# Optimization experiments

Hardware: AMD Instinct MI355X
Metric: run time of the kernel (lower is better)

The kernel has to match this reference:

```python
import jax, jax.numpy as jnp
import numpy as np

N_NODES = 10000
N_EDGES = 160000
F = 128
NRB = 32


def setup_inputs() -> dict:
    key = jax.random.key(0)
    ks = jax.random.split(key, 20)
    inp = {
        "s": jax.random.normal(ks[0], (N_NODES, F), jnp.float32),
        "v": jax.random.normal(ks[1], (N_NODES, 3, F), jnp.float32),
        "radial_embeddings_1": jax.random.normal(ks[2], (N_EDGES, NRB), jnp.float32),
        "radial_embeddings_2": jax.random.normal(ks[3], (N_EDGES, NRB), jnp.float32),
        "radial_embeddings_3": jax.random.normal(ks[4], (N_EDGES, NRB), jnp.float32),
        "f_cut_1": jax.random.uniform(ks[5], (N_EDGES,), jnp.float32),
        "f_cut_2": jax.random.uniform(ks[6], (N_EDGES,), jnp.float32),
        "f_cut_3": jax.random.uniform(ks[7], (N_EDGES,), jnp.float32),
        "unit_vectors_1": jax.random.normal(ks[8], (N_EDGES, 3), jnp.float32),
        "unit_vectors_2": jax.random.normal(ks[9], (N_EDGES, 3), jnp.float32),
        "unit_vectors_3": jax.random.normal(ks[10], (N_EDGES, 3), jnp.float32),
        "edge_index": jax.random.randint(ks[11], (2, N_EDGES), 0, N_NODES, jnp.int64),
    }
    # parameters (Linear uses y = x @ W.T + b; we store transposed for x @ W)
    sc1 = 1.0 / np.sqrt(F)
    sc2 = 1.0 / np.sqrt(NRB)
    inp["W1"] = jax.random.uniform(ks[12], (F, F), jnp.float32, -sc1, sc1)
    inp["b1"] = jax.random.uniform(ks[13], (F,), jnp.float32, -sc1, sc1)
    inp["W2"] = jax.random.uniform(ks[14], (F, 8 * F), jnp.float32, -sc1, sc1)
    inp["b2"] = jax.random.uniform(ks[15], (8 * F,), jnp.float32, -sc1, sc1)
    inp["Wr"] = jax.random.uniform(ks[16], (NRB, 8 * F), jnp.float32, -sc2, sc2)
    inp["br"] = jax.random.uniform(ks[17], (8 * F,), jnp.float32, -sc2, sc2)
    return inp


def reference(s, v, radial_embeddings_1, radial_embeddings_2, radial_embeddings_3,
              f_cut_1, f_cut_2, f_cut_3,
              unit_vectors_1, unit_vectors_2, unit_vectors_3,
              edge_index, W1, b1, W2, b2, Wr, br):
    idx_i, idx_j = edge_index[0], edge_index[1]
    n_nodes = s.shape[0]
    nf = W1.shape[0]

    # phi = Linear(F,F) -> SiLU -> Linear(F,8F)   [N, 8F]
    phi = jax.nn.silu(s @ W1 + b1) @ W2 + b2

    # shared-weight radial filter over 3 branches  [E, 8F]
    W = ((radial_embeddings_1 @ Wr + br) * f_cut_1[:, None]
         + (radial_embeddings_2 @ Wr + br) * f_cut_2[:, None]
         + (radial_embeddings_3 @ Wr + br) * f_cut_3[:, None])

    x = phi[idx_j] * W                                    # [E, 8F]
    x_s, x_vv, x_vs1, x_vs2, x_vs3, x_vc1, x_vc2, x_vc3 = jnp.split(x, 8, axis=-1)

    ds = jax.ops.segment_sum(x_s, idx_i, num_segments=n_nodes)

    vj = v[idx_j]                                         # [E, 3, F]
    ex = lambda a: a[:, None, :]                          # [E,1,F] broadcast over xyz
    cr = lambda u: jnp.cross(vj, u[..., None], axis=1)    # [E, 3, F]

    x_v = (vj * ex(x_vv)
           + ex(x_vs1) * unit_vectors_1[..., None]
           + ex(x_vs2) * unit_vectors_2[..., None]
           + ex(x_vs3) * unit_vectors_3[..., None]
           + ex(x_vc1) * cr(unit_vectors_1)
           + ex(x_vc2) * cr(unit_vectors_2)
           + ex(x_vc3) * cr(unit_vectors_3))              # [E, 3, F]

    dv = jax.ops.segment_sum(x_v, idx_i, num_segments=n_nodes)
    return (s + ds, v + dv)
```

## Files before the change

kernel.cpp:

```cpp
#include <hip/hip_runtime.h>

#define N_NODES 10000
#define N_EDGES 160000
#define MAXT     20000
#define MSG_GRID 5000

typedef __attribute__((ext_vector_type(8))) __bf16 bf16x8;
typedef __attribute__((ext_vector_type(8))) unsigned short u16x8;
typedef __attribute__((ext_vector_type(4))) float f32x4;

static __device__ __forceinline__ unsigned short f2bf(float x) {
    union { float f; unsigned u; } un;
    un.f = x;
    unsigned r = un.u + 0x7fffu + ((un.u >> 16) & 1u);
    return (unsigned short)(r >> 16);
}

static __device__ __forceinline__ float bf2f(unsigned short h) {
    union { unsigned u; float f; } un;
    un.u = ((unsigned)h) << 16;
    return un.f;
}

__global__ __launch_bounds__(256) void init_kernel(
    const float* __restrict__ s, const float* __restrict__ v,
    const int* __restrict__ eix,
    const float* __restrict__ W1, const float* __restrict__ W2,
    const float* __restrict__ Wr,
    float* __restrict__ out0, float* __restrict__ out1,
    unsigned short* __restrict__ vbf2, int* __restrict__ cnt,
    unsigned short* __restrict__ W1T, unsigned short* __restrict__ W2T,
    unsigned short* __restrict__ WrT)
{
    int tid = blockIdx.x * 256 + threadIdx.x;
    if (tid < N_NODES * 384) out1[tid] = v[tid];
    if (tid < N_NODES * 128) {
        out0[tid] = s[tid];
        int n = tid >> 7, f = tid & 127;
        ushort4 q;
        q.x = f2bf(v[(size_t)n * 384 + f]);
        q.y = f2bf(v[(size_t)n * 384 + 128 + f]);
        q.z = f2bf(v[(size_t)n * 384 + 256 + f]);
        q.w = 0;
        *reinterpret_cast<ushort4*>(vbf2 + (size_t)tid * 4) = q;
    }
    if (tid < 131072) {
        int n = tid >> 7, k = tid & 127;
        W2T[tid] = f2bf(W2[k * 1024 + n]);
    }
    if (tid < 16384) {
        int n = tid >> 7, k = tid & 127;
        W1T[tid] = f2bf(W1[k * 128 + n]);
    }
    if (tid < 32768) {
        int n = tid >> 5, k = tid & 31;
        WrT[tid] = f2bf(Wr[k * 1024 + n]);
    }
    if (tid < N_EDGES) atomicAdd(&cnt[eix[tid]], 1);
}

__global__ __launch_bounds__(1024) void scan_kernel(
    const int* __restrict__ cnt, int* __restrict__ cursor,
    int* __restrict__ tile_node, int* __restrict__ tile_e0,
    int* __restrict__ tile_cnt, int* __restrict__ ntiles)
{
    __shared__ int ws0[16], ws1[16];
    __shared__ int run0_s, run1_s;
    int t = threadIdx.x, lane = t & 63, wid = t >> 6;
    if (t == 0) { run0_s = 0; run1_s = 0; }
    __syncthreads();
    for (int base = 0; base < N_NODES; base += 1024) {
        int idx = base + t;
        int deg = (idx < N_NODES) ? cnt[idx] : 0;
        int tc = (deg + 15) >> 4;
        int x0 = deg, x1 = tc;
        #pragma unroll
        for (int o = 1; o < 64; o <<= 1) {
            int y0 = __shfl_up(x0, o), y1 = __shfl_up(x1, o);
            if (lane >= o) { x0 += y0; x1 += y1; }
        }
        if (lane == 63) { ws0[wid] = x0; ws1[wid] = x1; }
        __syncthreads();
        if (wid == 0) {
            int w0 = (lane < 16) ? ws0[lane] : 0;
            int w1 = (lane < 16) ? ws1[lane] : 0;
            #pragma unroll
            for (int o = 1; o < 16; o <<= 1) {
                int y0 = __shfl_up(w0, o), y1 = __shfl_up(w1, o);
                if (lane >= o) { w0 += y0; w1 += y1; }
            }
            if (lane < 16) { ws0[lane] = w0; ws1[lane] = w1; }
        }
        __syncthreads();
        int wb0 = wid ? ws0[wid - 1] : 0;
        int wb1 = wid ? ws1[wid - 1] : 0;
        int ex0 = run0_s + wb0 + x0 - deg;
        int ex1 = run1_s + wb1 + x1 - tc;
        if (idx < N_NODES) {
            cursor[idx] = ex0;
            for (int k = 0; k < tc; ++k) {
                tile_node[ex1 + k] = idx;
                tile_e0[ex1 + k]   = ex0 + k * 16;
                int rem = deg - k * 16;
                tile_cnt[ex1 + k]  = rem < 16 ? rem : 16;
            }
        }
        __syncthreads();
        if (t == 0) { run0_s += ws0[15]; run1_s += ws1[15]; }
        __syncthreads();
    }
    if (t == 0) *ntiles = run1_s;
}

__global__ __launch_bounds__(256) void rc_kernel(
    const float* __restrict__ R1, const float* __restrict__ R2,
    const float* __restrict__ R3,
    const float* __restrict__ f1, const float* __restrict__ f2,
    const float* __restrict__ f3,
    const int* __restrict__ eix, int* __restrict__ cursor,
    unsigned short* __restrict__ Rc, float* __restrict__ fsum,
    int* __restrict__ elist)
{
    int tid = blockIdx.x * 256 + threadIdx.x;
    int e = tid >> 3, sub = tid & 7;
    if (e >= N_EDGES) return;
    float a = f1[e], b = f2[e], c = f3[e];
    int k0 = sub * 4;
    float4 r1 = *reinterpret_cast<const float4*>(R1 + (size_t)e * 32 + k0);
    float4 r2 = *reinterpret_cast<const float4*>(R2 + (size_t)e * 32 + k0);
    float4 r3 = *reinterpret_cast<const float4*>(R3 + (size_t)e * 32 + k0);
    ushort4 o;
    o.x = f2bf(r1.x * a + r2.x * b + r3.x * c);
    o.y = f2bf(r1.y * a + r2.y * b + r3.y * c);
    o.z = f2bf(r1.z * a + r2.z * b + r3.z * c);
    o.w = f2bf(r1.w * a + r2.w * b + r3.w * c);
    *reinterpret_cast<ushort4*>(Rc + (size_t)e * 32 + k0) = o;
    if (sub == 0) {
        fsum[e] = a + b + c;
        int slot = atomicAdd(&cursor[eix[e]], 1);
        elist[slot] = e;
    }
}

__global__ __launch_bounds__(256) void phi_kernel(
    const float* __restrict__ s, const unsigned short* __restrict__ W1T,
    const float* __restrict__ b1, const unsigned short* __restrict__ W2T,
    const float* __restrict__ b2, unsigned short* __restrict__ phi2)
{
    __shared__ unsigned short h_lds[64][136];
    int t = threadIdx.x, lane = t & 63, w = t >> 6;
    int quad = lane >> 4, l16 = lane & 15;
    int m0 = (blockIdx.x >> 2) * 64;
    int colg = blockIdx.x & 3;

    int arow = m0 + w * 16 + l16;
    if (arow > N_NODES - 1) arow = N_NODES - 1;
    bf16x8 afr[4];
    #pragma unroll
    for (int ks = 0; ks < 4; ++ks) {
        const float* sp = s + (size_t)arow * 128 + ks * 32 + quad * 8;
        #pragma unroll
        for (int jj = 0; jj < 8; ++jj) afr[ks][jj] = (__bf16)sp[jj];
    }
    #pragma unroll
    for (int cg = 0; cg < 8; ++cg) {
        int col = cg * 16 + l16;
        f32x4 acc = {0.f, 0.f, 0.f, 0.f};
        #pragma unroll
        for (int ks = 0; ks < 4; ++ks) {
            bf16x8 bf = *reinterpret_cast<const bf16x8*>(W1T + (size_t)col * 128 + ks * 32 + quad * 8);
            acc = __builtin_amdgcn_mfma_f32_16x16x32_bf16(afr[ks], bf, acc, 0, 0, 0);
        }
        float bb = b1[col];
        #pragma unroll
        for (int r = 0; r < 4; ++r) {
            int row = w * 16 + quad * 4 + r;
            float val = acc[r] + bb;
            h_lds[row][col] = f2bf(val / (1.f + __expf(-val)));
        }
    }
    __syncthreads();

    bf16x8 a2[4][4];
    #pragma unroll
    for (int rg = 0; rg < 4; ++rg)
        #pragma unroll
        for (int ks = 0; ks < 4; ++ks)
            a2[rg][ks] = *reinterpret_cast<const bf16x8*>(&h_lds[rg * 16 + l16][ks * 32 + quad * 8]);
    #pragma unroll
    for (int i = 0; i < 4; ++i) {
        int col = colg * 256 + w * 64 + i * 16 + l16;
        f32x4 acc2[4] = {{0,0,0,0},{0,0,0,0},{0,0,0,0},{0,0,0,0}};
        #pragma unroll
        for (int ks = 0; ks < 4; ++ks) {
            bf16x8 bf = *reinterpret_cast<const bf16x8*>(W2T + (size_t)col * 128 + ks * 32 + quad * 8);
            #pragma unroll
            for (int rg = 0; rg < 4; ++rg)
                acc2[rg] = __builtin_amdgcn_mfma_f32_16x16x32_bf16(a2[rg][ks], bf, acc2[rg], 0, 0, 0);
        }
        float bb = b2[col];
        int f = col & 127, cc = col >> 7;
        #pragma unroll
        for (int rg = 0; rg < 4; ++rg)
            #pragma unroll
            for (int r = 0; r < 4; ++r) {
                int row = m0 + rg * 16 + quad * 4 + r;
                if (row < N_NODES)
                    phi2[(size_t)row * 1024 + f * 8 + cc] = f2bf(acc2[rg][r] + bb);
            }
    }
}

__global__ __launch_bounds__(512) void msg_kernel(
    const unsigned short* __restrict__ Rc, const float* __restrict__ fsum,
    const int* __restrict__ eix,
    const unsigned short* __restrict__ phi2, const unsigned short* __restrict__ vbf2,
    const unsigned short* __restrict__ WrT, const float* __restrict__ br,
    const int* __restrict__ elist,
    const int* __restrict__ tile_node, const int* __restrict__ tile_e0,
    const int* __restrict__ tile_cnt, const int* __restrict__ ntiles,
    const float* __restrict__ u1, const float* __restrict__ u2,
    const float* __restrict__ u3,
    float* __restrict__ out0, float* __restrict__ out1)
{
    int t = threadIdx.x, lane = t & 63, w = t >> 6;
    int quad = lane >> 4, l16 = lane & 15;
    int fcol = w * 16 + l16;
    const int nt = *ntiles;
    const int* idx_j = eix + N_EDGES;

    bf16x8 bfrag[8];
    float brv[8];
    #pragma unroll
    for (int c = 0; c < 8; ++c) {
        int col = c * 128 + fcol;
        bfrag[c] = *reinterpret_cast<const bf16x8*>(WrT + (size_t)col * 32 + quad * 8);
        brv[c] = br[col];
    }

    __shared__ float srow[2][16][12];

    for (int t4 = 0; t4 < 4; ++t4) {
        int tile = blockIdx.x + t4 * MSG_GRID;
        if (tile >= nt) break;
        int node = tile_node[tile], e0 = tile_e0[tile], tcnt = tile_cnt[tile];
        int p = t4 & 1;

        if (t < 192) {
            int row = t / 12, c = t - row * 12;
            float val = 0.f;
            if (row < tcnt) {
                int eid = elist[e0 + row];
                if (c == 0)      val = __int_as_float(idx_j[eid]);
                else if (c == 1) val = fsum[eid];
                else if (c < 5)  val = u1[(size_t)eid * 3 + c - 2];
                else if (c < 8)  val = u2[(size_t)eid * 3 + c - 5];
                else if (c < 11) val = u3[(size_t)eid * 3 + c - 8];
            }
            srow[p][row][c] = val;
        }

        int er = e0 + (l16 < tcnt ? l16 : 0);
        int eid_a = elist[er];
        bf16x8 af;
        if (l16 < tcnt)
            af = *reinterpret_cast<const bf16x8*>(Rc + (size_t)eid_a * 32 + quad * 8);
        else {
            #pragma unroll
            for (int q = 0; q < 8; ++q) af[q] = (__bf16)0.f;
        }

        f32x4 acc[8];
        #pragma unroll
        for (int c = 0; c < 8; ++c) {
            f32x4 z = {0.f, 0.f, 0.f, 0.f};
            acc[c] = __builtin_amdgcn_mfma_f32_16x16x32_bf16(af, bfrag[c], z, 0, 0, 0);
        }

        __syncthreads();

        float ds = 0.f, d0 = 0.f, d1 = 0.f, d2 = 0.f;
        #pragma unroll
        for (int r = 0; r < 4; ++r) {
            int row = quad * 4 + r;
            int j = __float_as_int(srow[p][row][0]);
            float fs = srow[p][row][1];
            u16x8 ph = *reinterpret_cast<const u16x8*>(phi2 + ((size_t)j * 128 + fcol) * 8);
            ushort4 vb = *reinterpret_cast<const ushort4*>(vbf2 + ((size_t)j * 128 + fcol) * 4);
            float x[8];
            #pragma unroll
            for (int c = 0; c < 8; ++c)
                x[c] = bf2f(ph[c]) * (acc[c][r] + brv[c] * fs);
            float vjx = bf2f(vb.x), vjy = bf2f(vb.y), vjz = bf2f(vb.z);
            float u1x = srow[p][row][2], u1y = srow[p][row][3], u1z = srow[p][row][4];
            float u2x = srow[p][row][5], u2y = srow[p][row][6], u2z = srow[p][row][7];
            float u3x = srow[p][row][8], u3y = srow[p][row][9], u3z = srow[p][row][10];

            ds += x[0];
            d0 += vjx * x[1] + u1x * x[2] + u2x * x[3] + u3x * x[4]
                + x[5] * (vjy * u1z - vjz * u1y)
                + x[6] * (vjy * u2z - vjz * u2y)
                + x[7] * (vjy * u3z - vjz * u3y);
            d1 += vjy * x[1] + u1y * x[2] + u2y * x[3] + u3y * x[4]
                + x[5] * (vjz * u1x - vjx * u1z)
                + x[6] * (vjz * u2x - vjx * u2z)
                + x[7] * (vjz * u3x - vjx * u3z);
            d2 += vjz * x[1] + u1z * x[2] + u2z * x[3] + u3z * x[4]
                + x[5] * (vjx * u1y - vjy * u1x)
                + x[6] * (vjx * u2y - vjy * u2x)
                + x[7] * (vjx * u3y - vjy * u3x);
        }

        ds += __shfl_xor(ds, 16); ds += __shfl_xor(ds, 32);
        d0 += __shfl_xor(d0, 16); d0 += __shfl_xor(d0, 32);
        d1 += __shfl_xor(d1, 16); d1 += __shfl_xor(d1, 32);
        d2 += __shfl_xor(d2, 16); d2 += __shfl_xor(d2, 32);

        if (quad == 0) {
            atomicAdd(&out0[(size_t)node * 128 + fcol], ds);
            size_t vo = (size_t)node * 384 + fcol;
            atomicAdd(&out1[vo], d0);
            atomicAdd(&out1[vo + 128], d1);
            atomicAdd(&out1[vo + 256], d2);
        }
    }
}

extern "C" void kernel_launch(void* const* d_in, const int* in_sizes, int n_in,
                              void* d_out, int out_size, void* d_ws, size_t ws_size,
                              hipStream_t stream) {
    const float* s  = (const float*)d_in[0];
    const float* v  = (const float*)d_in[1];
    const float* R1 = (const float*)d_in[2];
    const float* R2 = (const float*)d_in[3];
    const float* R3 = (const float*)d_in[4];
    const float* f1 = (const float*)d_in[5];
    const float* f2 = (const float*)d_in[6];
    const float* f3 = (const float*)d_in[7];
    const float* u1 = (const float*)d_in[8];
    const float* u2 = (const float*)d_in[9];
    const float* u3 = (const float*)d_in[10];
    const int*  eix = (const int*)d_in[11];
    const float* W1 = (const float*)d_in[12];
    const float* b1 = (const float*)d_in[13];
    const float* W2 = (const float*)d_in[14];
    const float* b2 = (const float*)d_in[15];
    const float* Wr = (const float*)d_in[16];
    const float* br = (const float*)d_in[17];

    char* ws = (char*)d_ws;
    size_t off = 0;
    auto alloc = [&](size_t bytes) -> void* {
        void* p = ws + off;
        off = (off + bytes + 255) & ~(size_t)255;
        return p;
    };
    int* cnt       = (int*)alloc((size_t)N_NODES * 4);
    int* cursor    = (int*)alloc((size_t)N_NODES * 4);
    int* tile_node = (int*)alloc((size_t)MAXT * 4);
    int* tile_e0   = (int*)alloc((size_t)MAXT * 4);
    int* tile_cnt  = (int*)alloc((size_t)MAXT * 4);
    int* ntiles    = (int*)alloc(4);
    int* elist     = (int*)alloc((size_t)N_EDGES * 4);
    unsigned short* Rc   = (unsigned short*)alloc((size_t)N_EDGES * 32 * 2);
    float* fsum          = (float*)alloc((size_t)N_EDGES * 4);
    unsigned short* vbf2 = (unsigned short*)alloc((size_t)N_NODES * 128 * 4 * 2);
    unsigned short* phi2 = (unsigned short*)alloc((size_t)N_NODES * 1024 * 2);
    unsigned short* W1T  = (unsigned short*)alloc(128 * 128 * 2);
    unsigned short* W2T  = (unsigned short*)alloc(1024 * 128 * 2);
    unsigned short* WrT  = (unsigned short*)alloc(1024 * 32 * 2);
    (void)ws_size; (void)in_sizes; (void)n_in; (void)out_size;

    float* out0 = (float*)d_out;
    float* out1 = out0 + (size_t)N_NODES * 128;

    hipMemsetAsync(cnt, 0, (size_t)N_NODES * 4, stream);
    init_kernel<<<15000, 256, 0, stream>>>(s, v, eix, W1, W2, Wr,
                                           out0, out1, vbf2, cnt, W1T, W2T, WrT);
    scan_kernel<<<1, 1024, 0, stream>>>(cnt, cursor, tile_node, tile_e0, tile_cnt, ntiles);
    rc_kernel<<<5000, 256, 0, stream>>>(R1, R2, R3, f1, f2, f3, eix, cursor,
                                        Rc, fsum, elist);
    phi_kernel<<<628, 256, 0, stream>>>(s, W1T, b1, W2T, b2, phi2);
    msg_kernel<<<MSG_GRID, 512, 0, stream>>>(Rc, fsum, eix, phi2, vbf2, WrT, br,
                                             elist, tile_node, tile_e0, tile_cnt,
                                             ntiles, u1, u2, u3, out0, out1);
}
```

Before: 366.8 us.

## Make msg kernel warp-independent, fold residual add into first tile, single-pass scan

The message kernel changes from 512-thread blocks that share one tile to 256-thread blocks in which each wavefront owns its own feature slice and grid-strides over tiles on its own. This removes __syncthreads and lets edge metadata be gathered through shuffles into per-wave shared memory. The s and v copies into the output are dropped in favour of a memset, and the residual is added by the first tile of each node, which is why every node now gets at least one tile. The scan becomes one pass with 10 nodes per thread. In exchange, each wave gathers edge metadata separately, duplicating that work 8 times per tile, and zero-degree nodes now produce tiles that do nothing but add the residual.

```diff
diff --git a/kernel.cpp b/kernel.cpp
--- a/kernel.cpp
+++ b/kernel.cpp
@@ -2,8 +2,8 @@
 
 #define N_NODES 10000
 #define N_EDGES 160000
-#define MAXT     20000
-#define MSG_GRID 5000
+#define MAXT     22000
+#define MSG_BLOCKS 4096
 
 typedef __attribute__((ext_vector_type(8))) __bf16 bf16x8;
 typedef __attribute__((ext_vector_type(8))) unsigned short u16x8;
@@ -22,20 +22,16 @@
     return un.f;
 }
 
-__global__ __launch_bounds__(256) void init_kernel(
-    const float* __restrict__ s, const float* __restrict__ v,
-    const int* __restrict__ eix,
+__global__ __launch_bounds__(256) void weights_kernel(
+    const float* __restrict__ v, const int* __restrict__ eix,
     const float* __restrict__ W1, const float* __restrict__ W2,
     const float* __restrict__ Wr,
-    float* __restrict__ out0, float* __restrict__ out1,
     unsigned short* __restrict__ vbf2, int* __restrict__ cnt,
     unsigned short* __restrict__ W1T, unsigned short* __restrict__ W2T,
     unsigned short* __restrict__ WrT)
 {
     int tid = blockIdx.x * 256 + threadIdx.x;
-    if (tid < N_NODES * 384) out1[tid] = v[tid];
     if (tid < N_NODES * 128) {
-        out0[tid] = s[tid];
         int n = tid >> 7, f = tid & 127;
         ushort4 q;
         q.x = f2bf(v[(size_t)n * 384 + f]);
@@ -59,57 +55,61 @@
     if (tid < N_EDGES) atomicAdd(&cnt[eix[tid]], 1);
 }
 
+#define NPT 10
 __global__ __launch_bounds__(1024) void scan_kernel(
     const int* __restrict__ cnt, int* __restrict__ cursor,
     int* __restrict__ tile_node, int* __restrict__ tile_e0,
     int* __restrict__ tile_cnt, int* __restrict__ ntiles)
 {
     __shared__ int ws0[16], ws1[16];
-    __shared__ int run0_s, run1_s;
     int t = threadIdx.x, lane = t & 63, wid = t >> 6;
-    if (t == 0) { run0_s = 0; run1_s = 0; }
+    int n0 = t * NPT;
+    int deg[NPT], tc[NPT];
+    int D = 0, T = 0;
+    #pragma unroll
+    for (int i = 0; i < NPT; ++i) {
+        int idx = n0 + i;
+        int d = (idx < N_NODES) ? cnt[idx] : 0;
+        deg[i] = d;
+        tc[i] = (idx < N_NODES) ? (d ? ((d + 15) >> 4) : 1) : 0;
+        D += d; T += tc[i];
+    }
+    int x0 = D, x1 = T;
+    #pragma unroll
+    for (int o = 1; o < 64; o <<= 1) {
+        int y0 = __shfl_up(x0, o), y1 = __shfl_up(x1, o);
+        if (lane >= o) { x0 += y0; x1 += y1; }
+    }
+    if (lane == 63) { ws0[wid] = x0; ws1[wid] = x1; }
     __syncthreads();
-    for (int base = 0; base < N_NODES; base += 1024) {
-        int idx = base + t;
-        int deg = (idx < N_NODES) ? cnt[idx] : 0;
-        int tc = (deg + 15) >> 4;
-        int x0 = deg, x1 = tc;
-        #pragma unroll
-        for (int o = 1; o < 64; o <<= 1) {
-            int y0 = __shfl_up(x0, o), y1 = __shfl_up(x1, o);
-            if (lane >= o) { x0 += y0; x1 += y1; }
-        }
-        if (lane == 63) { ws0[wid] = x0; ws1[wid] = x1; }
-        __syncthreads();
-        if (wid == 0) {
-            int w0 = (lane < 16) ? ws0[lane] : 0;
-            int w1 = (lane < 16) ? ws1[lane] : 0;
-            #pragma unroll
-            for (int o = 1; o < 16; o <<= 1) {
-                int y0 = __shfl_up(w0, o), y1 = __shfl_up(w1, o);
-                if (lane >= o) { w0 += y0; w1 += y1; }
+    if (wid == 0) {
+        int w0 = (lane < 16) ? ws0[lane] : 0;
+        int w1 = (lane < 16) ? ws1[lane] : 0;
+        #pragma unroll
+        for (int o = 1; o < 16; o <<= 1) {
+            int y0 = __shfl_up(w0, o), y1 = __shfl_up(w1, o);
+            if (lane >= o) { w0 += y0; w1 += y1; }
+        }
+        if (lane < 16) { ws0[lane] = w0; ws1[lane] = w1; }
+    }
+    __syncthreads();
+    int e0 = (wid ? ws0[wid - 1] : 0) + x0 - D;
+    int t0 = (wid ? ws1[wid - 1] : 0) + x1 - T;
+    #pragma unroll
+    for (int i = 0; i < NPT; ++i) {
+        int idx = n0 + i;
+        if (idx < N_NODES) {
+            cursor[idx] = e0;
+            for (int k = 0; k < tc[i]; ++k) {
+                tile_node[t0 + k] = (idx << 1) | (k == 0);
+                tile_e0[t0 + k]   = e0 + k * 16;
+                int rem = deg[i] - k * 16;
+                tile_cnt[t0 + k]  = rem < 0 ? 0 : (rem < 16 ? rem : 16);
             }
-            if (lane < 16) { ws0[lane] = w0; ws1[lane] = w1; }
-        }
-        __syncthreads();
-        int wb0 = wid ? ws0[wid - 1] : 0;
-        int wb1 = wid ? ws1[wid - 1] : 0;
-        int ex0 = run0_s + wb0 + x0 - deg;
-        int ex1 = run1_s + wb1 + x1 - tc;
-        if (idx < N_NODES) {
-            cursor[idx] = ex0;
-            for (int k = 0; k < tc; ++k) {
-                tile_node[ex1 + k] = idx;
-                tile_e0[ex1 + k]   = ex0 + k * 16;
-                int rem = deg - k * 16;
-                tile_cnt[ex1 + k]  = rem < 16 ? rem : 16;
-            }
-        }
-        __syncthreads();
-        if (t == 0) { run0_s += ws0[15]; run1_s += ws1[15]; }
-        __syncthreads();
-    }
-    if (t == 0) *ntiles = run1_s;
+            e0 += deg[i]; t0 += tc[i];
+        }
+    }
+    if (t == 1023) *ntiles = t0;
 }
 
 __global__ __launch_bounds__(256) void rc_kernel(
@@ -211,7 +211,7 @@
     }
 }
 
-__global__ __launch_bounds__(512) void msg_kernel(
+__global__ __launch_bounds__(256) void msg_kernel(
     const unsigned short* __restrict__ Rc, const float* __restrict__ fsum,
     const int* __restrict__ eix,
     const unsigned short* __restrict__ phi2, const unsigned short* __restrict__ vbf2,
@@ -221,13 +221,20 @@
     const int* __restrict__ tile_cnt, const int* __restrict__ ntiles,
     const float* __restrict__ u1, const float* __restrict__ u2,
     const float* __restrict__ u3,
+    const float* __restrict__ s, const float* __restrict__ v,
     float* __restrict__ out0, float* __restrict__ out1)
 {
-    int t = threadIdx.x, lane = t & 63, w = t >> 6;
+    __shared__ float srow[4][16][12];
+    int t = threadIdx.x, lane = t & 63, wid = t >> 6;
+    int gw = blockIdx.x * 4 + wid;
+    int w = gw & 7;
+    int tile0 = gw >> 3;
+    int tstride = (MSG_BLOCKS * 4) >> 3;
     int quad = lane >> 4, l16 = lane & 15;
     int fcol = w * 16 + l16;
+    const int* idx_j = eix + N_EDGES;
     const int nt = *ntiles;
-    const int* idx_j = eix + N_EDGES;
+    float* sw = &srow[wid][0][0];
 
     bf16x8 bfrag[8];
     float brv[8];
@@ -238,34 +245,36 @@
         brv[c] = br[col];
     }
 
-    __shared__ float srow[2][16][12];
-
-    for (int t4 = 0; t4 < 4; ++t4) {
-        int tile = blockIdx.x + t4 * MSG_GRID;
-        if (tile >= nt) break;
-        int node = tile_node[tile], e0 = tile_e0[tile], tcnt = tile_cnt[tile];
-        int p = t4 & 1;
-
-        if (t < 192) {
-            int row = t / 12, c = t - row * 12;
+    for (int tile = tile0; tile < nt; tile += tstride) {
+        int meta = tile_node[tile];
+        int node = meta >> 1, first = meta & 1;
+        int e0 = tile_e0[tile], tcnt = tile_cnt[tile];
+
+        int eid0 = 0;
+        if (lane < 16 && tcnt > 0)
+            eid0 = elist[e0 + (lane < tcnt ? lane : 0)];
+
+        #pragma unroll
+        for (int k = 0; k < 3; ++k) {
+            int vid = lane * 3 + k;
+            int row = vid / 12, c = vid - row * 12;
+            int eid = __shfl(eid0, row);
             float val = 0.f;
             if (row < tcnt) {
-                int eid = elist[e0 + row];
                 if (c == 0)      val = __int_as_float(idx_j[eid]);
                 else if (c == 1) val = fsum[eid];
                 else if (c < 5)  val = u1[(size_t)eid * 3 + c - 2];
                 else if (c < 8)  val = u2[(size_t)eid * 3 + c - 5];
                 else if (c < 11) val = u3[(size_t)eid * 3 + c - 8];
             }
-            srow[p][row][c] = val;
-        }
-
-        int er = e0 + (l16 < tcnt ? l16 : 0);
-        int eid_a = elist[er];
+            sw[vid] = val;
+        }
+
+        int eidA = __shfl(eid0, l16);
         bf16x8 af;
-        if (l16 < tcnt)
-            af = *reinterpret_cast<const bf16x8*>(Rc + (size_t)eid_a * 32 + quad * 8);
-        else {
+        if (l16 < tcnt) {
+            af = *reinterpret_cast<const bf16x8*>(Rc + (size_t)eidA * 32 + quad * 8);
+        } else {
             #pragma unroll
             for (int q = 0; q < 8; ++q) af[q] = (__bf16)0.f;
         }
@@ -277,14 +286,13 @@
             acc[c] = __builtin_amdgcn_mfma_f32_16x16x32_bf16(af, bfrag[c], z, 0, 0, 0);
         }
 
-        __syncthreads();
-
         float ds = 0.f, d0 = 0.f, d1 = 0.f, d2 = 0.f;
         #pragma unroll
         for (int r = 0; r < 4; ++r) {
             int row = quad * 4 + r;
-            int j = __float_as_int(srow[p][row][0]);
-            float fs = srow[p][row][1];
+            const float* sr = sw + row * 12;
+            int j = __float_as_int(sr[0]);
+            float fs = sr[1];
             u16x8 ph = *reinterpret_cast<const u16x8*>(phi2 + ((size_t)j * 128 + fcol) * 8);
             ushort4 vb = *reinterpret_cast<const ushort4*>(vbf2 + ((size_t)j * 128 + fcol) * 4);
             float x[8];
@@ -292,9 +300,9 @@
             for (int c = 0; c < 8; ++c)
                 x[c] = bf2f(ph[c]) * (acc[c][r] + brv[c] * fs);
             float vjx = bf2f(vb.x), vjy = bf2f(vb.y), vjz = bf2f(vb.z);
-            float u1x = srow[p][row][2], u1y = srow[p][row][3], u1z = srow[p][row][4];
-            float u2x = srow[p][row][5], u2y = srow[p][row][6], u2z = srow[p][row][7];
-            float u3x = srow[p][row][8], u3y = srow[p][row][9], u3z = srow[p][row][10];
+            float u1x = sr[2], u1y = sr[3], u1z = sr[4];
+            float u2x = sr[5], u2y = sr[6], u2z = sr[7];
+            float u3x = sr[8], u3y = sr[9], u3z = sr[10];
 
             ds += x[0];
             d0 += vjx * x[1] + u1x * x[2] + u2x * x[3] + u3x * x[4]
@@ -317,11 +325,18 @@
         d2 += __shfl_xor(d2, 16); d2 += __shfl_xor(d2, 32);
 
         if (quad == 0) {
-            atomicAdd(&out0[(size_t)node * 128 + fcol], ds);
-            size_t vo = (size_t)node * 384 + fcol;
-            atomicAdd(&out1[vo], d0);
-            atomicAdd(&out1[vo + 128], d1);
-            atomicAdd(&out1[vo + 256], d2);
+            size_t sbase = (size_t)node * 128 + fcol;
+            size_t vbase = (size_t)node * 384 + fcol;
+            if (first) {
+                ds += s[sbase];
+                d0 += v[vbase];
+                d1 += v[vbase + 128];
+                d2 += v[vbase + 256];
+            }
+            atomicAdd(&out0[sbase], ds);
+            atomicAdd(&out1[vbase], d0);
+            atomicAdd(&out1[vbase + 128], d1);
+            atomicAdd(&out1[vbase + 256], d2);
         }
     }
 }
@@ -369,19 +384,20 @@
     unsigned short* W1T  = (unsigned short*)alloc(128 * 128 * 2);
     unsigned short* W2T  = (unsigned short*)alloc(1024 * 128 * 2);
     unsigned short* WrT  = (unsigned short*)alloc(1024 * 32 * 2);
-    (void)ws_size; (void)in_sizes; (void)n_in; (void)out_size;
+    (void)ws_size; (void)in_sizes; (void)n_in;
 
     float* out0 = (float*)d_out;
     float* out1 = out0 + (size_t)N_NODES * 128;
 
     hipMemsetAsync(cnt, 0, (size_t)N_NODES * 4, stream);
-    init_kernel<<<15000, 256, 0, stream>>>(s, v, eix, W1, W2, Wr,
-                                           out0, out1, vbf2, cnt, W1T, W2T, WrT);
+    hipMemsetAsync(d_out, 0, (size_t)out_size * 4, stream);
+    weights_kernel<<<5000, 256, 0, stream>>>(v, eix, W1, W2, Wr,
+                                             vbf2, cnt, W1T, W2T, WrT);
     scan_kernel<<<1, 1024, 0, stream>>>(cnt, cursor, tile_node, tile_e0, tile_cnt, ntiles);
     rc_kernel<<<5000, 256, 0, stream>>>(R1, R2, R3, f1, f2, f3, eix, cursor,
                                         Rc, fsum, elist);
     phi_kernel<<<628, 256, 0, stream>>>(s, W1T, b1, W2T, b2, phi2);
-    msg_kernel<<<MSG_GRID, 512, 0, stream>>>(Rc, fsum, eix, phi2, vbf2, WrT, br,
-                                             elist, tile_node, tile_e0, tile_cnt,
-                                             ntiles, u1, u2, u3, out0, out1);
-}
+    msg_kernel<<<MSG_BLOCKS, 256, 0, stream>>>(Rc, fsum, eix, phi2, vbf2, WrT, br,
+                                               elist, tile_node, tile_e0, tile_cnt,
+                                               ntiles, u1, u2, u3, s, v, out0, out1);
+}
```

After: 481.7 us. 1.31x slower.
